# Optimization experiments

Hardware: AMD Instinct MI355X
Metric: run time of the kernel (lower is better)

The kernel has to match this reference:

```python
import jax, jax.numpy as jnp
import numpy as np

L = 4        # num_layers
H = 1024     # hidden_size
NH = 16      # num_heads
KVH = 4      # num_kv_heads
QPK = NH // KVH
HD = H // NH # head_dim = 64
FF = 4096    # intermediate_size
V = 32000    # vocab_size
B, S = 2, 2048
EPS = 1e-5
STD = 0.02


def layernorm(x, g, b):
    m = jnp.mean(x, axis=-1, keepdims=True)
    v = jnp.mean(jnp.square(x - m), axis=-1, keepdims=True)
    return (x - m) * jax.lax.rsqrt(v + EPS) * g + b


def setup_inputs() -> dict:
    key = jax.random.key(0)
    ks = iter(jax.random.split(key, 24))
    n = lambda shape: STD * jax.random.normal(next(ks), shape, dtype=jnp.float32)
    KV = H * KVH // NH  # kv_size = 256
    inp = {
        'input_ids': jax.random.randint(next(ks), (B, S), 0, V),
        'attention_mask': jnp.zeros((B, S), dtype=jnp.float32),
        'tok_emb': n((V, H)),
        'pos_emb': n((S, H)),
        # per-layer stacked weights, stored [in, out] so y = x @ W + b
        'Wq': n((L, H, H)),  'bq': jnp.zeros((L, H)),
        'Wk': n((L, H, KV)), 'bk': jnp.zeros((L, KV)),
        'Wv': n((L, H, KV)), 'bv': jnp.zeros((L, KV)),
        'Wo': n((L, H, H)),  'bo': jnp.zeros((L, H)),
        'W1': n((L, H, FF)), 'b1': jnp.zeros((L, FF)),
        'W2': n((L, FF, H)), 'b2': jnp.zeros((L, H)),
        'ln1_g': jnp.ones((L, H)), 'ln1_b': jnp.zeros((L, H)),
        'ln2_g': jnp.ones((L, H)), 'ln2_b': jnp.zeros((L, H)),
        'lnf_g': jnp.ones((H,)),   'lnf_b': jnp.zeros((H,)),
        'Whead': n((H, V)),  # head has no bias
    }
    return inp


def gpt_forward(input_ids, attention_mask, tok_emb, pos_emb,
                Wq, bq, Wk, bk, Wv, bv, Wo, bo,
                W1, b1, W2, b2, ln1_g, ln1_b, ln2_g, ln2_b,
                lnf_g, lnf_b, Whead):
    b, s = input_ids.shape
    x = tok_emb[input_ids] + pos_emb[None, :s, :]  # [b,s,H]
    mask = attention_mask[:, None, None, None, :]  # [b,1,1,1,s] additive
    scale = 1.0 / jnp.sqrt(jnp.float32(HD))
    for l in range(L):
        h = layernorm(x, ln1_g[l], ln1_b[l])
        q = h @ Wq[l] + bq[l]                              # [b,s,H]
        k = h @ Wk[l] + bk[l]                              # [b,s,KV]
        v = h @ Wv[l] + bv[l]
        q = q.reshape(b, s, KVH, QPK, HD).transpose(0, 2, 3, 1, 4)  # [b,g,q,s,d]
        k = k.reshape(b, s, KVH, HD).transpose(0, 2, 1, 3)          # [b,g,s,d]
        v = v.reshape(b, s, KVH, HD).transpose(0, 2, 1, 3)
        scores = jnp.einsum('bgqsd,bgkd->bgqsk', q, k) * scale      # [b,g,q,s,s]
        scores = scores + mask
        w = jax.nn.softmax(scores, axis=-1)
        o = jnp.einsum('bgqsk,bgkd->bgqsd', w, v)                   # [b,g,q,s,d]
        o = o.transpose(0, 3, 1, 2, 4).reshape(b, s, H)
        x = x + (o @ Wo[l] + bo[l])
        h2 = layernorm(x, ln2_g[l], ln2_b[l])
        ff = jax.nn.gelu(h2 @ W1[l] + b1[l], approximate=False) @ W2[l] + b2[l]
        x = x + ff
    x = layernorm(x, lnf_g, lnf_b)
    return x @ Whead  # [b,s,V] logits


def reference(input_ids, attention_mask, tok_emb, pos_emb,
              Wq, bq, Wk, bk, Wv, bv, Wo, bo,
              W1, b1, W2, b2, ln1_g, ln1_b, ln2_g, ln2_b,
              lnf_g, lnf_b, Whead):
    return gpt_forward(input_ids, attention_mask, tok_emb, pos_emb,
                       Wq, bq, Wk, bk, Wv, bv, Wo, bo,
                       W1, b1, W2, b2, ln1_g, ln1_b, ln2_g, ln2_b,
                       lnf_g, lnf_b, Whead)
```

## Files before the change

kernel.cpp:

```cpp
#include <hip/hip_runtime.h>
#include <hip/hip_bf16.h>

#define LAYERS 4
#define H 1024
#define NH 16
#define KVH 4
#define HD 64
#define KVD 256
#define FF 4096
#define VOC 32000
#define BB 2
#define SS 2048
#define MROWS (BB*SS)
#define QKVN 1536

typedef __attribute__((ext_vector_type(4))) float f32x4;
typedef __attribute__((ext_vector_type(8))) short short8;
typedef __attribute__((ext_vector_type(4))) unsigned short u16x4;
typedef __attribute__((ext_vector_type(2))) unsigned int u32x2;

__device__ inline unsigned short f2bf(float f){
  union { float f; unsigned u; } v; v.f = f;
  return (unsigned short)((v.u + 0x7FFFu + ((v.u >> 16) & 1u)) >> 16);
}
__device__ inline unsigned cvt_pk_bf16(float a, float b){
  unsigned r;
  asm("v_cvt_pk_bf16_f32 %0, %1, %2" : "=v"(r) : "v"(a), "v"(b));
  return r;
}

__global__ __launch_bounds__(256) void embed_kernel(const int* __restrict__ ids,
    const float* __restrict__ tok, const float* __restrict__ pos, float* __restrict__ x)
{
  int row = blockIdx.x;
  int s = row & (SS-1);
  int id = ids[row];
  int t = threadIdx.x;
  f32x4 a = *(const f32x4*)&tok[(size_t)id*H + t*4];
  f32x4 p = *(const f32x4*)&pos[(size_t)s*H + t*4];
  *(f32x4*)&x[(size_t)row*H + t*4] = a + p;
}

__global__ __launch_bounds__(256) void ln_kernel(const float* __restrict__ x,
    const float* __restrict__ g, const float* __restrict__ b, unsigned short* __restrict__ out)
{
  int row = blockIdx.x;
  int t = threadIdx.x;
  const float* xr = x + (size_t)row*H;
  f32x4 v = *(const f32x4*)&xr[t*4];
  float s  = v[0]+v[1]+v[2]+v[3];
  float s2 = v[0]*v[0]+v[1]*v[1]+v[2]*v[2]+v[3]*v[3];
  #pragma unroll
  for (int off=1; off<64; off<<=1){ s += __shfl_xor(s,off); s2 += __shfl_xor(s2,off); }
  __shared__ float red[8];
  int w = t>>6;
  if ((t&63)==0){ red[w]=s; red[4+w]=s2; }
  __syncthreads();
  float S1 = red[0]+red[1]+red[2]+red[3];
  float S2 = red[4]+red[5]+red[6]+red[7];
  float mean = S1 * (1.0f/H);
  float var  = S2 * (1.0f/H) - mean*mean;
  float rs = rsqrtf(var + 1e-5f);
  u16x4 o;
  #pragma unroll
  for (int i=0;i<4;i++) o[i] = f2bf((v[i]-mean)*rs*g[t*4+i] + b[t*4+i]);
  *(u16x4*)&out[(size_t)row*H + t*4] = o;
}

__global__ __launch_bounds__(256) void convT_kernel(const float* __restrict__ in,
    unsigned short* __restrict__ out, int K, int N, size_t istride, size_t ostride)
{
  __shared__ float t[32][33];
  in  += (size_t)blockIdx.z * istride;
  out += (size_t)blockIdx.z * ostride;
  int n0 = blockIdx.x*32, k0 = blockIdx.y*32;
  int x = threadIdx.x & 31, y = threadIdx.x >> 5;
  #pragma unroll
  for (int j=0;j<4;j++) t[y+j*8][x] = in[(size_t)(k0+y+j*8)*N + n0 + x];
  __syncthreads();
  int x2 = threadIdx.x & 15, y2 = threadIdx.x >> 4;
  #pragma unroll
  for (int j=0;j<2;j++){
    int n = y2 + j*16;
    unsigned lo = f2bf(t[x2*2][n]);
    unsigned hi = f2bf(t[x2*2+1][n]);
    *(unsigned*)&out[(size_t)(n0+n)*K + k0 + x2*2] = lo | (hi<<16);
  }
}

__global__ __launch_bounds__(256) void bcat_kernel(const float* __restrict__ bq,
    const float* __restrict__ bk, const float* __restrict__ bv, float* __restrict__ out)
{
  int l = blockIdx.x, t = threadIdx.x;
  #pragma unroll
  for (int i=0;i<4;i++) out[l*QKVN + t + i*256] = bq[l*H + t + i*256];
  out[l*QKVN + 1024 + t] = bk[l*KVD + t];
  out[l*QKVN + 1280 + t] = bv[l*KVD + t];
}

template<int EPI>
__global__ __launch_bounds__(256) void gemm_bt(
    const unsigned short* __restrict__ A, const unsigned short* __restrict__ Bt,
    const float* __restrict__ bias, const float* __restrict__ res,
    float* __restrict__ outf, unsigned short* __restrict__ outb,
    unsigned short* __restrict__ outb2, unsigned short* __restrict__ outb3, int N, int K)
{
  __shared__ unsigned short As[128*32];
  __shared__ unsigned short Bs[128*32];
  int m0 = blockIdx.x*128, n0 = blockIdx.y*128;
  int tid = threadIdx.x;
  int lane = tid & 63, w = tid >> 6;
  int wr = (w>>1)*64, wc = (w&1)*64;
  int fr = lane & 15, fq = lane >> 4;
  f32x4 acc[4][4] = {};
  int srow = lane >> 2;
  int scol = (lane & 3) * 8;
  const unsigned short* a0 = A  + (size_t)m0*K + scol;
  const unsigned short* b0 = Bt + (size_t)n0*K + scol;
  for (int k0 = 0; k0 < K; k0 += 32){
    __syncthreads();
    #pragma unroll
    for (int c = 0; c < 2; c++){
      int ch = w*2 + c;
      int row = ch*16 + srow;
      __builtin_amdgcn_global_load_lds(
        (const __attribute__((address_space(1))) void*)(a0 + (size_t)row*K + k0),
        (__attribute__((address_space(3))) void*)(As + ch*512), 16, 0, 0);
      __builtin_amdgcn_global_load_lds(
        (const __attribute__((address_space(1))) void*)(b0 + (size_t)row*K + k0),
        (__attribute__((address_space(3))) void*)(Bs + ch*512), 16, 0, 0);
    }
    __syncthreads();
    short8 af[4], bf[4];
    #pragma unroll
    for (int mi=0;mi<4;mi++) af[mi] = *(const short8*)&As[(wr+mi*16+fr)*32 + fq*8];
    #pragma unroll
    for (int ni=0;ni<4;ni++) bf[ni] = *(const short8*)&Bs[(wc+ni*16+fr)*32 + fq*8];
    #pragma unroll
    for (int mi=0;mi<4;mi++)
      #pragma unroll
      for (int ni=0;ni<4;ni++)
        acc[mi][ni] = __builtin_amdgcn_mfma_f32_16x16x32_bf16(af[mi], bf[ni], acc[mi][ni], 0,0,0);
  }
  #pragma unroll
  for (int mi=0;mi<4;mi++)
    #pragma unroll
    for (int ni=0;ni<4;ni++){
      int col = n0 + wc + ni*16 + fr;
      float bi = (EPI==3) ? 0.0f : bias[col];
      #pragma unroll
      for (int r=0;r<4;r++){
        int row = m0 + wr + mi*16 + fq*4 + r;
        float vv = acc[mi][ni][r] + bi;
        if (EPI==1)      { size_t idx=(size_t)row*N+col; outf[idx] = vv + res[idx]; }
        else if (EPI==2) { size_t idx=(size_t)row*N+col; outb[idx] = f2bf(0.5f*vv*(1.0f+erff(vv*0.70710678118f))); }
        else if (EPI==3) { size_t idx=(size_t)row*N+col; outf[idx] = vv; }
        else if (EPI==5) {
          if (col < 1024)      outb [(size_t)row*H + col]            = f2bf(vv);
          else if (col < 1280) outb2[(size_t)row*KVD + (col-1024)]   = f2bf(vv);
          else                 outb3[(size_t)(col-1280)*MROWS + row] = f2bf(vv);
        }
      }
    }
}

template<int EPI>
__global__ __launch_bounds__(512, 2) void gemm256(
    const unsigned short* __restrict__ A, const unsigned short* __restrict__ Bt,
    const float* __restrict__ bias, float* __restrict__ outf,
    unsigned short* __restrict__ outb, int N, int K)
{
  __shared__ __align__(16) char lds[131072];
  const int tid = threadIdx.x;
  const int lane = tid & 63, wid = tid >> 6;
  const int wr = wid >> 2, wc = wid & 3;
  const int fr = lane & 15, fq = lane >> 4;
  const int m0 = blockIdx.x*256, n0 = blockIdx.y*256;
  const int nt = K >> 5;
  f32x4 acc[8][4] = {};

  const int srl = tid >> 2;
  const int ssl = tid & 3;

  #define STAGE(bb, kt) do {                                                     \
    int k0e = (kt)*32;                                                           \
    _Pragma("unroll")                                                            \
    for (int hh=0; hh<2; hh++){                                                  \
      int rr = hh*128 + srl;                                                     \
      int sc = ssl ^ ((rr>>1)&3);                                                \
      __builtin_amdgcn_global_load_lds(                                          \
        (const __attribute__((address_space(1))) void*)(A + (size_t)(m0+rr)*K + k0e + sc*8), \
        (__attribute__((address_space(3))) void*)(lds + (bb)*32768 + hh*8192 + wid*1024), 16, 0, 0); \
    }                                                                            \
    _Pragma("unroll")                                                            \
    for (int hh=0; hh<2; hh++){                                                  \
      int rr = hh*128 + srl;                                                     \
      int sc = ssl ^ ((rr>>1)&3);                                                \
      __builtin_amdgcn_global_load_lds(                                          \
        (const __attribute__((address_space(1))) void*)(Bt + (size_t)(n0+rr)*K + k0e + sc*8), \
        (__attribute__((address_space(3))) void*)(lds + (bb)*32768 + 16384 + hh*8192 + wid*1024), 16, 0, 0); \
    }                                                                            \
  } while(0)

  STAGE(0, 0);
  STAGE(1, 1);
  asm volatile("s_waitcnt vmcnt(4)" ::: "memory");
  __builtin_amdgcn_s_barrier();

  for (int t = 0; t < nt; ++t){
    const int c = t & 3;
    const char* ab = lds + c*32768;
    const char* bb_ = lds + c*32768 + 16384;
    short8 bf[4], af[4];
    #pragma unroll
    for (int ni=0; ni<4; ni++){
      int r = wc*64 + ni*16 + fr;
      bf[ni] = *(const short8*)(bb_ + r*64 + ((fq ^ ((r>>1)&3))*16));
    }
    #pragma unroll
    for (int mi=0; mi<4; mi++){
      int r = wr*128 + mi*16 + fr;
      af[mi] = *(const short8*)(ab + r*64 + ((fq ^ ((r>>1)&3))*16));
    }
    {
      int t2 = t + 2;
      int kt = (t2 < nt) ? t2 : (nt-1);
      STAGE(t2 & 3, kt);
    }
    __builtin_amdgcn_s_barrier();
    __builtin_amdgcn_s_setprio(1);
    #pragma unroll
    for (int mi=0; mi<4; mi++)
      #pragma unroll
      for (int ni=0; ni<4; ni++)
        acc[mi][ni] = __builtin_amdgcn_mfma_f32_16x16x32_bf16(af[mi], bf[ni], acc[mi][ni], 0,0,0);
    __builtin_amdgcn_s_setprio(0);
    __builtin_amdgcn_s_barrier();
    short8 ag[4];
    #pragma unroll
    for (int mi=0; mi<4; mi++){
      int r = wr*128 + (4+mi)*16 + fr;
      ag[mi] = *(const short8*)(ab + r*64 + ((fq ^ ((r>>1)&3))*16));
    }
    asm volatile("s_waitcnt vmcnt(4)" ::: "memory");
    __builtin_amdgcn_s_barrier();
    __builtin_amdgcn_s_setprio(1);
    #pragma unroll
    for (int mi=0; mi<4; mi++)
      #pragma unroll
      for (int ni=0; ni<4; ni++)
        acc[4+mi][ni] = __builtin_amdgcn_mfma_f32_16x16x32_bf16(ag[mi], bf[ni], acc[4+mi][ni], 0,0,0);
    __builtin_amdgcn_s_setprio(0);
    __builtin_amdgcn_s_barrier();
  }
  #undef STAGE

  #pragma unroll
  for (int mi=0; mi<8; mi++)
    #pragma unroll
    for (int ni=0; ni<4; ni++){
      int col = n0 + wc*64 + ni*16 + fr;
      float bi = (EPI==3) ? 0.0f : bias[col];
      #pragma unroll
      for (int r=0; r<4; r++){
        int row = m0 + wr*128 + mi*16 + fq*4 + r;
        float vv = acc[mi][ni][r] + bi;
        size_t idx = (size_t)row*N + col;
        if (EPI==3) outf[idx] = vv;
        else        outb[idx] = f2bf(0.5f*vv*(1.0f+erff(vv*0.70710678118f)));
      }
    }
}

#define LOG2E 1.4426950408889634f
__global__ __launch_bounds__(256) void attn_kernel(
    const unsigned short* __restrict__ q, const unsigned short* __restrict__ kptr,
    const unsigned short* __restrict__ vt, const float* __restrict__ mask,
    unsigned short* __restrict__ o)
{
  __shared__ char Pbuf[4][4096];
  int tid = threadIdx.x;
  int lane = tid & 63, wid = tid >> 6;
  int fr = lane & 15, fq = lane >> 4, fo = fq*8;
  int h = blockIdx.y, b = blockIdx.z, g = h >> 2;
  int qcol = h*HD, kcol = g*HD;
  int qbase = b*SS + blockIdx.x*128 + wid*32;
  char* Pl = Pbuf[wid];
  int swz = (fr & 7) << 4;

  short8 bq[2][2];
  #pragma unroll
  for (int h2=0; h2<2; h2++){
    const unsigned short* qrow = q + (size_t)(qbase + h2*16 + fr)*H + qcol;
    bq[h2][0] = *(const short8*)(qrow + fo);
    bq[h2][1] = *(const short8*)(qrow + 32 + fo);
  }

  f32x4 oacc[2][4] = {};
  float mrun[2] = {-1e30f, -1e30f}, lsum[2] = {0.f, 0.f};
  const float sc2 = 0.125f * LOG2E;

  const unsigned short* kp[4];
  #pragma unroll
  for (int f=0; f<4; f++) kp[f] = kptr + (size_t)(b*SS + f*16 + fr)*KVD + kcol + fo;
  const unsigned short* vp[4];
  #pragma unroll
  for (int dc=0; dc<4; dc++) vp[dc] = vt + (size_t)(kcol + dc*16 + fr)*MROWS + b*SS + fo;
  const float* mp = mask + b*SS + fq*4;

  short8 kaA[4][2], kaB[4][2];
  #pragma unroll
  for (int f=0; f<4; f++){
    kaA[f][0] = *(const short8*)(kp[f]);
    kaA[f][1] = *(const short8*)(kp[f] + 32);
    kp[f] += 64*KVD;
  }

#define ATTN_STEP(KA, KB, PF) do {                                             \
    f32x4 mkv[4];                                                              \
    _Pragma("unroll")                                                          \
    for (int f=0; f<4; f++) mkv[f] = *(const f32x4*)(mp + f*16);               \
    short8 va[4][2];                                                           \
    _Pragma("unroll")                                                          \
    for (int dc=0; dc<4; dc++){                                                \
      va[dc][0] = *(const short8*)(vp[dc]);                                    \
      va[dc][1] = *(const short8*)(vp[dc] + 32);                               \
    }                                                                          \
    f32x4 sf[2][4] = {};                                                       \
    __builtin_amdgcn_s_setprio(1);                                             \
    _Pragma("unroll")                                                          \
    for (int h2=0; h2<2; h2++)                                                 \
      _Pragma("unroll")                                                        \
      for (int f=0; f<4; f++){                                                 \
        sf[h2][f] = __builtin_amdgcn_mfma_f32_16x16x32_bf16(KA[f][0], bq[h2][0], sf[h2][f],0,0,0); \
        sf[h2][f] = __builtin_amdgcn_mfma_f32_16x16x32_bf16(KA[f][1], bq[h2][1], sf[h2][f],0,0,0); \
      }                                                                        \
    __builtin_amdgcn_s_setprio(0);                                             \
    if (PF){                                                                   \
      _Pragma("unroll")                                                        \
      for (int f=0; f<4; f++){                                                 \
        KB[f][0] = *(const short8*)(kp[f]);                                    \
        KB[f][1] = *(const short8*)(kp[f] + 32);                               \
        kp[f] += 64*KVD;                                                       \
      }                                                                        \
    }                                                                          \
    _Pragma("unroll")                                                          \
    for (int f=0; f<4; f++){                                                   \
      _Pragma("unroll")                                                        \
      for (int r=0; r<4; r++){                                                 \
        float m2 = mkv[f][r]*LOG2E;                                            \
        sf[0][f][r] = sf[0][f][r]*sc2 + m2;                                    \
        sf[1][f][r] = sf[1][f][r]*sc2 + m2;                                    \
      }                                                                        \
    }                                                                          \
    float pm[2];                                                               \
    _Pragma("unroll")                                                          \
    for (int h2=0; h2<2; h2++){                                                \
      float a0 = fmaxf(fmaxf(sf[h2][0][0],sf[h2][0][1]), fmaxf(sf[h2][0][2],sf[h2][0][3])); \
      float a1 = fmaxf(fmaxf(sf[h2][1][0],sf[h2][1][1]), fmaxf(sf[h2][1][2],sf[h2][1][3])); \
      float a2 = fmaxf(fmaxf(sf[h2][2][0],sf[h2][2][1]), fmaxf(sf[h2][2][2],sf[h2][2][3])); \
      float a3 = fmaxf(fmaxf(sf[h2][3][0],sf[h2][3][1]), fmaxf(sf[h2][3][2],sf[h2][3][3])); \
      float p = fmaxf(fmaxf(a0,a1), fmaxf(a2,a3));                             \
      p = fmaxf(p, __shfl_xor(p, 16));                                         \
      p = fmaxf(p, __shfl_xor(p, 32));                                         \
      pm[h2] = p;                                                              \
    }                                                                          \
    if (!__all(pm[0] <= mrun[0]+8.f && pm[1] <= mrun[1]+8.f)){                 \
      float al[2];                                                             \
      _Pragma("unroll")                                                        \
      for (int h2=0; h2<2; h2++){                                              \
        float mn = fmaxf(mrun[h2], pm[h2]);                                    \
        al[h2] = __builtin_amdgcn_exp2f(mrun[h2]-mn);                          \
        mrun[h2] = mn;                                                         \
        lsum[h2] *= al[h2];                                                    \
      }                                                                        \
      _Pragma("unroll")                                                        \
      for (int r=0; r<4; r++){                                                 \
        float altl = __shfl(al[0], fq*4+r);                                    \
        float alth = __shfl(al[1], fq*4+r);                                    \
        _Pragma("unroll")                                                      \
        for (int dc=0; dc<4; dc++){ oacc[0][dc][r]*=altl; oacc[1][dc][r]*=alth; } \
      }                                                                        \
    }                                                                          \
    _Pragma("unroll")                                                          \
    for (int h2=0; h2<2; h2++){                                                \
      float ps = 0.f;                                                          \
      _Pragma("unroll")                                                        \
      for (int f=0; f<4; f++)                                                  \
        _Pragma("unroll")                                                      \
        for (int r=0; r<4; r++){                                               \
          float e = __builtin_amdgcn_exp2f(sf[h2][f][r]-mrun[h2]);             \
          sf[h2][f][r] = e; ps += e;                                           \
        }                                                                      \
      ps += __shfl_xor(ps, 16);                                                \
      ps += __shfl_xor(ps, 32);                                                \
      lsum[h2] += ps;                                                          \
    }                                                                          \
    _Pragma("unroll")                                                          \
    for (int h2=0; h2<2; h2++){                                                \
      int prow = h2*16 + fr;                                                   \
      _Pragma("unroll")                                                        \
      for (int f=0; f<4; f++){                                                 \
        u32x2 pw;                                                              \
        pw[0] = cvt_pk_bf16(sf[h2][f][0], sf[h2][f][1]);                       \
        pw[1] = cvt_pk_bf16(sf[h2][f][2], sf[h2][f][3]);                       \
        *(u32x2*)(Pl + prow*128 + ((f*32 + fq*8) ^ swz)) = pw;                 \
      }                                                                        \
    }                                                                          \
    __builtin_amdgcn_s_setprio(1);                                             \
    _Pragma("unroll")                                                          \
    for (int h2=0; h2<2; h2++){                                                \
      int prow = h2*16 + fr;                                                   \
      _Pragma("unroll")                                                        \
      for (int gs=0; gs<2; gs++){                                              \
        short8 pa = *(const short8*)(Pl + prow*128 + ((gs*64 + fq*16) ^ swz)); \
        _Pragma("unroll")                                                      \
        for (int dc=0; dc<4; dc++)                                             \
          oacc[h2][dc] = __builtin_amdgcn_mfma_f32_16x16x32_bf16(pa, va[dc][gs], oacc[h2][dc],0,0,0); \
      }                                                                        \
    }                                                                          \
    __builtin_amdgcn_s_setprio(0);                                             \
    _Pragma("unroll")                                                          \
    for (int dc=0; dc<4; dc++) vp[dc] += 64;                                   \
    mp += 64;                                                                  \
  } while(0)

  for (int it = 0; it < SS/128 - 1; ++it){
    ATTN_STEP(kaA, kaB, 1);
    ATTN_STEP(kaB, kaA, 1);
  }
  ATTN_STEP(kaA, kaB, 1);
  ATTN_STEP(kaB, kaA, 0);
#undef ATTN_STEP

  #pragma unroll
  for (int h2=0; h2<2; h2++){
    float lt[4];
    #pragma unroll
    for (int r=0; r<4; r++) lt[r] = __shfl(lsum[h2], fq*4+r);
    #pragma unroll
    for (int dc=0; dc<4; dc++)
      #pragma unroll
      for (int r=0; r<4; r++){
        int row = qbase + h2*16 + fq*4 + r;
        o[(size_t)row*H + qcol + dc*16 + fr] = f2bf(oacc[h2][dc][r] / lt[r]);
      }
  }
}

extern "C" void kernel_launch(void* const* d_in, const int* in_sizes, int n_in,
                              void* d_out, int out_size, void* d_ws, size_t ws_size,
                              hipStream_t stream)
{
  const int*   ids  = (const int*)  d_in[0];
  const float* mask = (const float*)d_in[1];
  const float* tok  = (const float*)d_in[2];
  const float* pos  = (const float*)d_in[3];
  const float* Wq   = (const float*)d_in[4];
  const float* bq   = (const float*)d_in[5];
  const float* Wk   = (const float*)d_in[6];
  const float* bk   = (const float*)d_in[7];
  const float* Wv   = (const float*)d_in[8];
  const float* bv   = (const float*)d_in[9];
  const float* Wo   = (const float*)d_in[10];
  const float* bo   = (const float*)d_in[11];
  const float* W1   = (const float*)d_in[12];
  const float* b1   = (const float*)d_in[13];
  const float* W2   = (const float*)d_in[14];
  const float* b2   = (const float*)d_in[15];
  const float* ln1g = (const float*)d_in[16];
  const float* ln1b = (const float*)d_in[17];
  const float* ln2g = (const float*)d_in[18];
  const float* ln2b = (const float*)d_in[19];
  const float* lnfg = (const float*)d_in[20];
  const float* lnfb = (const float*)d_in[21];
  const float* Wh   = (const float*)d_in[22];
  float* out = (float*)d_out;

  char* ws = (char*)d_ws;
  float*          x    = (float*)ws;          ws += (size_t)MROWS*H*4;
  unsigned short* hb   = (unsigned short*)ws; ws += (size_t)MROWS*H*2;
  unsigned short* qb   = (unsigned short*)ws; ws += (size_t)MROWS*H*2;
  unsigned short* kb   = (unsigned short*)ws; ws += (size_t)MROWS*KVD*2;
  unsigned short* vtb  = (unsigned short*)ws; ws += (size_t)KVD*MROWS*2;
  unsigned short* ob   = (unsigned short*)ws; ws += (size_t)MROWS*H*2;
  unsigned short* f1   = (unsigned short*)ws; ws += (size_t)MROWS*FF*2;
  unsigned short* Wqkv = (unsigned short*)ws; ws += (size_t)LAYERS*QKVN*H*2;
  unsigned short* WoT  = (unsigned short*)ws; ws += (size_t)LAYERS*H*H*2;
  unsigned short* W1T  = (unsigned short*)ws; ws += (size_t)LAYERS*H*FF*2;
  unsigned short* W2T  = (unsigned short*)ws; ws += (size_t)LAYERS*H*FF*2;
  unsigned short* WhT  = (unsigned short*)ws; ws += (size_t)H*VOC*2;
  float*          bcat = (float*)ws;          ws += (size_t)LAYERS*QKVN*4;

  convT_kernel<<<dim3(H/32,   H/32,  LAYERS), 256, 0, stream>>>(Wq, Wqkv,          H,  H,   (size_t)H*H,   (size_t)QKVN*H);
  convT_kernel<<<dim3(KVD/32, H/32,  LAYERS), 256, 0, stream>>>(Wk, Wqkv + 1024*H, H,  KVD, (size_t)H*KVD, (size_t)QKVN*H);
  convT_kernel<<<dim3(KVD/32, H/32,  LAYERS), 256, 0, stream>>>(Wv, Wqkv + 1280*H, H,  KVD, (size_t)H*KVD, (size_t)QKVN*H);
  convT_kernel<<<dim3(H/32,   H/32,  LAYERS), 256, 0, stream>>>(Wo, WoT,           H,  H,   (size_t)H*H,   (size_t)H*H);
  convT_kernel<<<dim3(FF/32,  H/32,  LAYERS), 256, 0, stream>>>(W1, W1T,           H,  FF,  (size_t)H*FF,  (size_t)H*FF);
  convT_kernel<<<dim3(H/32,   FF/32, LAYERS), 256, 0, stream>>>(W2, W2T,           FF, H,   (size_t)FF*H,  (size_t)FF*H);
  convT_kernel<<<dim3(VOC/32, H/32,  1),      256, 0, stream>>>(Wh, WhT,           H,  VOC, 0, 0);
  bcat_kernel<<<LAYERS, 256, 0, stream>>>(bq, bk, bv, bcat);

  embed_kernel<<<MROWS, 256, 0, stream>>>(ids, tok, pos, x);
  for (int l=0; l<LAYERS; l++){
    ln_kernel<<<MROWS,256,0,stream>>>(x, ln1g + l*H, ln1b + l*H, hb);
    gemm_bt<5><<<dim3(MROWS/128, QKVN/128),256,0,stream>>>(hb, Wqkv + (size_t)l*QKVN*H, bcat + l*QKVN, nullptr, nullptr, qb, kb, vtb, QKVN, H);
    attn_kernel<<<dim3(SS/128, NH, BB), 256, 0, stream>>>(qb, kb, vtb, mask, ob);
    gemm_bt<1><<<dim3(MROWS/128, H/128),  256,0,stream>>>(ob, WoT + (size_t)l*H*H,  bo + l*H,  x, x, nullptr, nullptr, nullptr, H, H);
    ln_kernel<<<MROWS,256,0,stream>>>(x, ln2g + l*H, ln2b + l*H, hb);
    gemm256<2><<<dim3(MROWS/256, FF/256), 512,0,stream>>>(hb, W1T + (size_t)l*H*FF, b1 + l*FF, nullptr, f1, FF, H);
    gemm_bt<1><<<dim3(MROWS/128, H/128),  256,0,stream>>>(f1, W2T + (size_t)l*H*FF, b2 + l*H,  x, x, nullptr, nullptr, nullptr, H, FF);
  }
  ln_kernel<<<MROWS,256,0,stream>>>(x, lnfg, lnfb, hb);
  gemm256<3><<<dim3(MROWS/256, VOC/256), 512,0,stream>>>(hb, WhT, nullptr, out, nullptr, VOC, H);
}
```

Measured before the change: 2.020 ms.

## Restructure gemm256 main loop into double-buffered 64-wide K steps with split staging

The 256x256 GEMM main loop now steps K by 64 per iteration using two LDS buffers, each holding two 32-wide halves, instead of a four-deep ring of 32-wide stages. Global-to-LDS loads for the next K step are split into four pieces, each issued between MFMA phases, with explicit lgkmcnt waits after each barrier. The aim is to interleave memory traffic more finely with compute and to halve loop overhead per K. In exchange the prefetch distance is shorter (one iteration ahead rather than two) and the loop has more barriers.

```diff
diff --git a/kernel.cpp b/kernel.cpp
--- a/kernel.cpp
+++ b/kernel.cpp
@@ -176,84 +176,96 @@
   const int wr = wid >> 2, wc = wid & 3;
   const int fr = lane & 15, fq = lane >> 4;
   const int m0 = blockIdx.x*256, n0 = blockIdx.y*256;
-  const int nt = K >> 5;
+  const int nt = K >> 6;
   f32x4 acc[8][4] = {};
 
-  const int srl = tid >> 2;
-  const int ssl = tid & 3;
-
-  #define STAGE(bb, kt) do {                                                     \
-    int k0e = (kt)*32;                                                           \
+  #define STAGEH(PTR, baserow, kt, kk, ldsoff) do {                              \
     _Pragma("unroll")                                                            \
-    for (int hh=0; hh<2; hh++){                                                  \
-      int rr = hh*128 + srl;                                                     \
-      int sc = ssl ^ ((rr>>1)&3);                                                \
+    for (int c=0;c<2;c++){                                                       \
+      int r = c*128 + (tid>>2);                                                  \
+      int ss = (tid&3) ^ ((r>>1)&3);                                             \
       __builtin_amdgcn_global_load_lds(                                          \
-        (const __attribute__((address_space(1))) void*)(A + (size_t)(m0+rr)*K + k0e + sc*8), \
-        (__attribute__((address_space(3))) void*)(lds + (bb)*32768 + hh*8192 + wid*1024), 16, 0, 0); \
-    }                                                                            \
-    _Pragma("unroll")                                                            \
-    for (int hh=0; hh<2; hh++){                                                  \
-      int rr = hh*128 + srl;                                                     \
-      int sc = ssl ^ ((rr>>1)&3);                                                \
-      __builtin_amdgcn_global_load_lds(                                          \
-        (const __attribute__((address_space(1))) void*)(Bt + (size_t)(n0+rr)*K + k0e + sc*8), \
-        (__attribute__((address_space(3))) void*)(lds + (bb)*32768 + 16384 + hh*8192 + wid*1024), 16, 0, 0); \
+        (const __attribute__((address_space(1))) void*)((PTR) + (size_t)((baserow)+r)*K + (kt)*64 + (kk)*32 + ss*8), \
+        (__attribute__((address_space(3))) void*)(lds + (ldsoff) + c*8192 + wid*1024), 16, 0, 0); \
     }                                                                            \
   } while(0)
 
-  STAGE(0, 0);
-  STAGE(1, 1);
+  #define RD_A(buf,kk,row) (*(const short8*)(lds + ((buf)*2+(kk))*16384 + (row)*64 + ((fq ^ (((row)>>1)&3))*16)))
+  #define RD_B(buf,kk,row) (*(const short8*)(lds + 65536 + ((buf)*2+(kk))*16384 + (row)*64 + ((fq ^ (((row)>>1)&3))*16)))
+
+  STAGEH(A,  m0, 0, 0, 0);
+  STAGEH(Bt, n0, 0, 0, 65536);
+  STAGEH(A,  m0, 0, 1, 16384);
+  STAGEH(Bt, n0, 0, 1, 65536+16384);
   asm volatile("s_waitcnt vmcnt(4)" ::: "memory");
   __builtin_amdgcn_s_barrier();
 
   for (int t = 0; t < nt; ++t){
-    const int c = t & 3;
-    const char* ab = lds + c*32768;
-    const char* bb_ = lds + c*32768 + 16384;
+    const int buf = t & 1, nb = buf ^ 1;
+    const int kt1 = (t+1 < nt) ? t+1 : t;
     short8 bf[4], af[4];
     #pragma unroll
-    for (int ni=0; ni<4; ni++){
-      int r = wc*64 + ni*16 + fr;
-      bf[ni] = *(const short8*)(bb_ + r*64 + ((fq ^ ((r>>1)&3))*16));
-    }
-    #pragma unroll
-    for (int mi=0; mi<4; mi++){
-      int r = wr*128 + mi*16 + fr;
-      af[mi] = *(const short8*)(ab + r*64 + ((fq ^ ((r>>1)&3))*16));
-    }
-    {
-      int t2 = t + 2;
-      int kt = (t2 < nt) ? t2 : (nt-1);
-      STAGE(t2 & 3, kt);
-    }
-    __builtin_amdgcn_s_barrier();
+    for (int ni=0;ni<4;ni++) bf[ni] = RD_B(buf,0, wc*64+ni*16+fr);
+    #pragma unroll
+    for (int mi=0;mi<4;mi++) af[mi] = RD_A(buf,0, wr*128+mi*16+fr);
+    STAGEH(A, m0, kt1, 0, (nb*2+0)*16384);
+    __builtin_amdgcn_s_barrier();
+    asm volatile("s_waitcnt lgkmcnt(0)" ::: "memory");
     __builtin_amdgcn_s_setprio(1);
     #pragma unroll
-    for (int mi=0; mi<4; mi++)
-      #pragma unroll
-      for (int ni=0; ni<4; ni++)
+    for (int mi=0;mi<4;mi++)
+      #pragma unroll
+      for (int ni=0;ni<4;ni++)
         acc[mi][ni] = __builtin_amdgcn_mfma_f32_16x16x32_bf16(af[mi], bf[ni], acc[mi][ni], 0,0,0);
     __builtin_amdgcn_s_setprio(0);
     __builtin_amdgcn_s_barrier();
-    short8 ag[4];
-    #pragma unroll
-    for (int mi=0; mi<4; mi++){
-      int r = wr*128 + (4+mi)*16 + fr;
-      ag[mi] = *(const short8*)(ab + r*64 + ((fq ^ ((r>>1)&3))*16));
-    }
+    #pragma unroll
+    for (int mi=0;mi<4;mi++) af[mi] = RD_A(buf,0, wr*128+(4+mi)*16+fr);
+    STAGEH(Bt, n0, kt1, 0, 65536+(nb*2+0)*16384);
+    __builtin_amdgcn_s_barrier();
+    asm volatile("s_waitcnt lgkmcnt(0)" ::: "memory");
+    __builtin_amdgcn_s_setprio(1);
+    #pragma unroll
+    for (int mi=0;mi<4;mi++)
+      #pragma unroll
+      for (int ni=0;ni<4;ni++)
+        acc[4+mi][ni] = __builtin_amdgcn_mfma_f32_16x16x32_bf16(af[mi], bf[ni], acc[4+mi][ni], 0,0,0);
+    __builtin_amdgcn_s_setprio(0);
     asm volatile("s_waitcnt vmcnt(4)" ::: "memory");
     __builtin_amdgcn_s_barrier();
+    #pragma unroll
+    for (int ni=0;ni<4;ni++) bf[ni] = RD_B(buf,1, wc*64+ni*16+fr);
+    #pragma unroll
+    for (int mi=0;mi<4;mi++) af[mi] = RD_A(buf,1, wr*128+mi*16+fr);
+    STAGEH(A, m0, kt1, 1, (nb*2+1)*16384);
+    __builtin_amdgcn_s_barrier();
+    asm volatile("s_waitcnt lgkmcnt(0)" ::: "memory");
     __builtin_amdgcn_s_setprio(1);
     #pragma unroll
-    for (int mi=0; mi<4; mi++)
-      #pragma unroll
-      for (int ni=0; ni<4; ni++)
-        acc[4+mi][ni] = __builtin_amdgcn_mfma_f32_16x16x32_bf16(ag[mi], bf[ni], acc[4+mi][ni], 0,0,0);
+    for (int mi=0;mi<4;mi++)
+      #pragma unroll
+      for (int ni=0;ni<4;ni++)
+        acc[mi][ni] = __builtin_amdgcn_mfma_f32_16x16x32_bf16(af[mi], bf[ni], acc[mi][ni], 0,0,0);
     __builtin_amdgcn_s_setprio(0);
     __builtin_amdgcn_s_barrier();
-  }
-  #undef STAGE
+    #pragma unroll
+    for (int mi=0;mi<4;mi++) af[mi] = RD_A(buf,1, wr*128+(4+mi)*16+fr);
+    STAGEH(Bt, n0, kt1, 1, 65536+(nb*2+1)*16384);
+    __builtin_amdgcn_s_barrier();
+    asm volatile("s_waitcnt lgkmcnt(0)" ::: "memory");
+    __builtin_amdgcn_s_setprio(1);
+    #pragma unroll
+    for (int mi=0;mi<4;mi++)
+      #pragma unroll
+      for (int ni=0;ni<4;ni++)
+        acc[4+mi][ni] = __builtin_amdgcn_mfma_f32_16x16x32_bf16(af[mi], bf[ni], acc[4+mi][ni], 0,0,0);
+    __builtin_amdgcn_s_setprio(0);
+    asm volatile("s_waitcnt vmcnt(4)" ::: "memory");
+    __builtin_amdgcn_s_barrier();
+  }
+  #undef STAGEH
+  #undef RD_A
+  #undef RD_B
 
   #pragma unroll
   for (int mi=0; mi<8; mi++)
```

After: 1.989 ms. About the same (-1.5%).
